# Optimization experiments

Hardware: AMD Instinct MI355X
Metric: run time of the kernel (lower is better)

## Reference

```python
import jax, jax.numpy as jnp
import numpy as np

B, T, E = 8, 1024, 512
H = 1024            # hidden_dim
NH, QD, VD = 4, 256, 512
C1, C2 = 512, 2     # conv1_out, conv2_out
K, PAD = 3, 1


def conv1d(x, w, b, pad):
    # x: [B, Cin, T], w: [Cout, Cin, K]
    y = jax.lax.conv_general_dilated(x, w, (1,), [(pad, pad)],
                                     dimension_numbers=('NCH', 'OIH', 'NCH'))
    return y + b[None, :, None]


def setup_inputs() -> dict:
    key = jax.random.key(0)
    ks = jax.random.split(key, 24)
    n = lambda i, shape, s=0.02: jax.random.normal(ks[i], shape, dtype=jnp.float32) * s
    inp = {
        'x':    jax.random.normal(ks[0], (B, T, E), dtype=jnp.float32),
        # in_pro: two 1x1 convs over channels (acting as linears)
        'w_in1': n(1, (E, E)), 'b_in1': jnp.zeros((E,), jnp.float32),
        'w_in2': n(2, (E, E)), 'b_in2': jnp.zeros((E,), jnp.float32),
        # attention projections
        'w_q': n(3, (NH * QD, E), float(np.sqrt(2.0 / (E + QD)))), 'b_q': jnp.zeros((NH * QD,), jnp.float32),
        'w_k': n(4, (NH * QD, E), float(np.sqrt(2.0 / (E + QD)))), 'b_k': jnp.zeros((NH * QD,), jnp.float32),
        'w_v': n(5, (NH * VD, E), float(np.sqrt(2.0 / (E + VD)))), 'b_v': jnp.zeros((NH * VD,), jnp.float32),
        # output projection (1x1 conv)
        'w_p': n(6, (E, NH * VD)), 'b_p': jnp.zeros((E,), jnp.float32),
        # layernorm
        'ln_g': jnp.ones((E,), jnp.float32), 'ln_b': jnp.zeros((E,), jnp.float32),
        # LSTM (1 layer, unidirectional, hidden H)
        'w_ih': n(7, (4 * H, E)), 'w_hh': n(8, (4 * H, H)),
        'b_ih': jnp.zeros((4 * H,), jnp.float32), 'b_hh': jnp.zeros((4 * H,), jnp.float32),
        # attention pooling convs
        'w_c1': n(9, (C1, H, K)), 'b_c1': jnp.zeros((C1,), jnp.float32),
        'w_c2': n(10, (C2, C1, K)), 'b_c2': jnp.zeros((C2,), jnp.float32),
    }
    return inp


def reference(x, w_in1, b_in1, w_in2, b_in2, w_q, b_q, w_k, b_k, w_v, b_v,
              w_p, b_p, ln_g, ln_b, w_ih, w_hh, b_ih, b_hh,
              w_c1, b_c1, w_c2, b_c2):
    # in_pro: 1x1 conv -> LeakyReLU(0.25) -> 1x1 conv (channel-wise linears)
    h = jnp.einsum('bte,fe->btf', x, w_in1) + b_in1
    h = jnp.where(h >= 0, h, 0.25 * h)
    h = jnp.einsum('bte,fe->btf', h, w_in2) + b_in2  # [B,T,E]

    # multi-head attention (no scale factor, as in the source)
    q = (jnp.einsum('bte,fe->btf', h, w_q) + b_q).reshape(B, T, NH, QD)
    k = (jnp.einsum('bte,fe->btf', h, w_k) + b_k).reshape(B, T, NH, QD)
    v = (jnp.einsum('bte,fe->btf', h, w_v) + b_v).reshape(B, T, NH, VD)
    scores = jnp.einsum('btnd,bsnd->bnts', q, k)          # [B,NH,T,T]
    attn = jax.nn.softmax(scores, axis=-1)
    o = jnp.einsum('bnts,bsnd->btnd', attn, v)            # [B,T,NH,VD]
    o = o.reshape(B, T, NH * VD)

    # p_conv1 (1x1) then LayerNorm over E
    y = jnp.einsum('btc,ec->bte', o, w_p) + b_p           # [B,T,E]
    mu = jnp.mean(y, axis=-1, keepdims=True)
    var = jnp.mean(jnp.square(y - mu), axis=-1, keepdims=True)
    y = (y - mu) * jax.lax.rsqrt(var + 1e-5) * ln_g + ln_b

    # LSTM (batch_first, 1 layer); dropout is identity in eval mode
    def step(carry, xt):
        hprev, cprev = carry
        g = xt @ w_ih.T + hprev @ w_hh.T + b_ih + b_hh    # [B,4H]
        i, f, gg, og = jnp.split(g, 4, axis=-1)
        c = jax.nn.sigmoid(f) * cprev + jax.nn.sigmoid(i) * jnp.tanh(gg)
        hn = jax.nn.sigmoid(og) * jnp.tanh(c)
        return (hn, c), hn
    init = (jnp.zeros((B, H), y.dtype), jnp.zeros((B, H), y.dtype))
    _, hs = jax.lax.scan(step, init, jnp.swapaxes(y, 0, 1))  # [T,B,H]
    lstm_out = jnp.swapaxes(hs, 0, 1)                        # [B,T,H]

    # conv-based attention pooling
    a = conv1d(jnp.swapaxes(lstm_out, 1, 2), w_c1, b_c1, PAD)  # [B,C1,T]
    a = jax.nn.relu(a)
    a = conv1d(a, w_c2, b_c2, PAD)                              # [B,C2,T]
    a = jax.nn.softmax(a, axis=2)
    feat = jnp.einsum('bct,bth->bch', a, lstm_out)              # [B,C2,H]
    return feat.reshape(B, C2 * H)
```

## Files before the change

### kernel.cpp

```cpp
#include <hip/hip_runtime.h>
#include <stdint.h>

typedef short short8 __attribute__((ext_vector_type(8)));
typedef short short4v __attribute__((ext_vector_type(4)));
typedef float float4v __attribute__((ext_vector_type(4)));

__device__ __forceinline__ float b2f(short s) {
    return __uint_as_float(((unsigned)(unsigned short)s) << 16);
}
__device__ __forceinline__ short f2b(float f) {
    unsigned u = __float_as_uint(f);
    unsigned r = (u + 0x7fffu + ((u >> 16) & 1u)) >> 16;
    return (short)r;
}

__global__ void k_prep_all(const float4v* __restrict__ xs,
                           const float4v* __restrict__ s0, const float4v* __restrict__ s1,
                           const float4v* __restrict__ s2, const float4v* __restrict__ s3,
                           const float4v* __restrict__ s4, const float4v* __restrict__ s5,
                           const float4v* __restrict__ s6, const float4v* __restrict__ s7,
                           short4v* __restrict__ xq, short4v* __restrict__ wq,
                           const float* __restrict__ wc1, short* __restrict__ wc1b,
                           const float* __restrict__ bih, const float* __restrict__ bhh,
                           float* __restrict__ bsum,
                           const float* __restrict__ bq, const float* __restrict__ bk,
                           const float* __restrict__ bv, float* __restrict__ bqkv,
                           short* __restrict__ lpad,
                           short* __restrict__ hs0, short* __restrict__ hs1,
                           int* __restrict__ arr, const float* __restrict__ bc2,
                           float* __restrict__ a2) {
    int t0 = blockIdx.x * blockDim.x + threadIdx.x;
    int stride = gridDim.x * blockDim.x;
    for (int i = t0; i < 3538944; i += stride) {
        float4v v;
        short4v* dst;
        int di;
        if (i < 1048576) { v = xs[i]; dst = xq; di = i; }
        else {
            int j = i - 1048576;
            dst = wq; di = j;
            if      (j <   65536) v = s0[j];
            else if (j <  131072) v = s1[j -   65536];
            else if (j <  262144) v = s2[j -  131072];
            else if (j <  393216) v = s3[j -  262144];
            else if (j <  655360) v = s4[j -  393216];
            else if (j <  917504) v = s5[j -  655360];
            else if (j < 1441792) v = s6[j -  917504];
            else                  v = s7[j - 1441792];
        }
        short4v o;
        o[0] = f2b(v[0]); o[1] = f2b(v[1]); o[2] = f2b(v[2]); o[3] = f2b(v[3]);
        dst[di] = o;
    }
    for (int i = t0; i < 512 * 3072; i += stride) {
        int c = i / 3072, rr = i % 3072, dk = rr / 1024, h = rr % 1024;
        wc1b[i] = f2b(wc1[(c * 1024 + h) * 3 + dk]);
    }
    for (int i = t0; i < 4096; i += stride) bsum[i] = bih[i] + bhh[i];
    for (int i = t0; i < 4096; i += stride) {
        float v;
        if (i < 1024) v = bq[i];
        else if (i < 2048) v = bk[i - 1024];
        else v = bv[i - 2048];
        bqkv[i] = v;
    }
    for (int i = t0; i < 16 * 1024; i += stride) {
        int b = i >> 11, r = (i >> 10) & 1, h = i & 1023;
        lpad[((long)(b * 1026 + r * 1025)) * 1024 + h] = 0;
    }
    for (int i = t0; i < 16384; i += stride) { hs0[i] = 0; hs1[i] = 0; }
    for (int i = t0; i < 64; i += stride) arr[i] = 0;
    for (int i = t0; i < 16384; i += stride) a2[i] = bc2[(i >> 10) & 1];
}

__global__ __launch_bounds__(256) void k_gemm_bt(
    const short* __restrict__ A, const short* __restrict__ B,
    float* __restrict__ Cf, short* __restrict__ Cb,
    const float* __restrict__ bias,
    int M, int N, int K, int lda, int ldb, int ldc,
    int z0n, long sA0, long sA1, long sB0, long sB1, long sC0, long sC1,
    int act, int gap, short* __restrict__ Cvt, int vtn0)
{
    __shared__ __align__(16) short lds[2 * 128 * 32];
    const int z = blockIdx.z;
    const int z0 = z % z0n, z1 = z / z0n;
    A += z1 * sA1 + z0 * sA0;
    B += z1 * sB1 + z0 * sB0;
    const long coff = z1 * sC1 + z0 * sC0;
    const int tn0 = blockIdx.x * 128, tm0 = blockIdx.y * 128;
    const int tid = threadIdx.x, ln = tid & 63, wv = tid >> 6;
    const int wr = wv >> 1, wc = wv & 1;

    const short* gbase[4];
    {
        const int gcol = (ln & 3) ^ ((ln >> 3) & 3);
#pragma unroll
        for (int j = 0; j < 4; ++j) {
            int c = wv * 4 + j;
            if (c < 8) {
                long grow = (long)(tm0 + c * 16 + (ln >> 2));
                if (gap) grow += 2 * (grow >> 10);
                gbase[j] = A + grow * (long)lda + gcol * 8;
            } else {
                gbase[j] = B + (long)(tn0 + (c - 8) * 16 + (ln >> 2)) * ldb + gcol * 8;
            }
        }
    }

    float4v acc[4][4];
#pragma unroll
    for (int i = 0; i < 4; ++i)
#pragma unroll
        for (int j = 0; j < 4; ++j) acc[i][j] = (float4v){0.f, 0.f, 0.f, 0.f};

    const int nk = K >> 5;
    for (int kt = 0; kt < nk; ++kt) {
        __syncthreads();
#pragma unroll
        for (int j = 0; j < 4; ++j) {
            int c = wv * 4 + j;
            __builtin_amdgcn_global_load_lds(
                (const __attribute__((address_space(1))) void*)(gbase[j] + kt * 32),
                (__attribute__((address_space(3))) void*)((short8*)lds + c * 64),
                16, 0, 0);
        }
        __syncthreads();

        short8 af[4], bf_[4];
        const int q = ln >> 4;
#pragma unroll
        for (int i = 0; i < 4; ++i) {
            int r = wr * 64 + i * 16 + (ln & 15);
            af[i] = ((short8*)lds)[r * 4 + (q ^ ((r >> 1) & 3))];
        }
#pragma unroll
        for (int j = 0; j < 4; ++j) {
            int r = wc * 64 + j * 16 + (ln & 15);
            bf_[j] = ((short8*)lds)[512 + r * 4 + (q ^ ((r >> 1) & 3))];
        }
#pragma unroll
        for (int i = 0; i < 4; ++i)
#pragma unroll
            for (int j = 0; j < 4; ++j)
                acc[i][j] = __builtin_amdgcn_mfma_f32_16x16x32_bf16(af[i], bf_[j], acc[i][j], 0, 0, 0);
    }

    if (Cvt && tn0 >= vtn0) {
#pragma unroll
        for (int j = 0; j < 4; ++j) {
            int nglob = tn0 + wc * 64 + j * 16 + (ln & 15);
            float bv = bias ? bias[nglob] : 0.f;
            int nv = nglob - vtn0;
            int nn = nv >> 9, d = nv & 511;
#pragma unroll
            for (int i = 0; i < 4; ++i) {
                int m0 = tm0 + wr * 64 + i * 16 + (ln >> 4) * 4;
                int b = m0 >> 10, s = m0 & 1023;
                short4v pk;
#pragma unroll
                for (int r = 0; r < 4; ++r) pk[r] = f2b(acc[i][j][r] + bv);
                *(short4v*)&Cvt[((long)((b * 4 + nn) * 512 + d)) * 1024 + s] = pk;
            }
        }
        return;
    }

#pragma unroll
    for (int j = 0; j < 4; ++j) {
        int nglob = tn0 + wc * 64 + j * 16 + (ln & 15);
        float bv = bias ? bias[nglob] : 0.f;
#pragma unroll
        for (int i = 0; i < 4; ++i) {
#pragma unroll
            for (int r = 0; r < 4; ++r) {
                int mglob = tm0 + wr * 64 + i * 16 + (ln >> 4) * 4 + r;
                float v = acc[i][j][r] + bv;
                if (act == 1) v = (v >= 0.f) ? v : 0.25f * v;
                else if (act == 2) v = fmaxf(v, 0.f);
                long ci = coff + (long)mglob * ldc + nglob;
                if (Cf) Cf[ci] = v;
                if (Cb) Cb[ci] = f2b(v);
            }
        }
    }
}

__global__ __launch_bounds__(256) void k_gemm_bt64(
    const short* __restrict__ A, const short* __restrict__ B,
    float* __restrict__ Cf, short* __restrict__ Cb,
    const float* __restrict__ bias,
    int M, int N, int K, int lda, int ldb, int ldc,
    int z0n, long sA0, long sA1, long sB0, long sB1, long sC0, long sC1,
    int act, int gap)
{
    __shared__ __align__(16) short lds[(64 + 128) * 32];
    const int z = blockIdx.z;
    const int z0 = z % z0n, z1 = z / z0n;
    A += z1 * sA1 + z0 * sA0;
    B += z1 * sB1 + z0 * sB0;
    const long coff = z1 * sC1 + z0 * sC0;
    const int tn0 = blockIdx.x * 128, tm0 = blockIdx.y * 64;
    const int tid = threadIdx.x, ln = tid & 63, wv = tid >> 6;
    const int wr = wv >> 1, wc = wv & 1;

    const short* gbase[3];
    {
        const int gcol = (ln & 3) ^ ((ln >> 3) & 3);
#pragma unroll
        for (int j = 0; j < 3; ++j) {
            int c = wv * 3 + j;
            if (c < 4) {
                long grow = (long)(tm0 + c * 16 + (ln >> 2));
                if (gap) grow += 2 * (grow >> 10);
                gbase[j] = A + grow * (long)lda + gcol * 8;
            } else {
                gbase[j] = B + (long)(tn0 + (c - 4) * 16 + (ln >> 2)) * ldb + gcol * 8;
            }
        }
    }

    float4v acc[2][4];
#pragma unroll
    for (int i = 0; i < 2; ++i)
#pragma unroll
        for (int j = 0; j < 4; ++j) acc[i][j] = (float4v){0.f, 0.f, 0.f, 0.f};

    const int nk = K >> 5;
    for (int kt = 0; kt < nk; ++kt) {
        __syncthreads();
#pragma unroll
        for (int j = 0; j < 3; ++j) {
            int c = wv * 3 + j;
            __builtin_amdgcn_global_load_lds(
                (const __attribute__((address_space(1))) void*)(gbase[j] + kt * 32),
                (__attribute__((address_space(3))) void*)((short8*)lds + c * 64),
                16, 0, 0);
        }
        __syncthreads();

        short8 af[2], bf_[4];
        const int q = ln >> 4;
#pragma unroll
        for (int i = 0; i < 2; ++i) {
            int r = wr * 32 + i * 16 + (ln & 15);
            af[i] = ((short8*)lds)[r * 4 + (q ^ ((r >> 1) & 3))];
        }
#pragma unroll
        for (int j = 0; j < 4; ++j) {
            int r = wc * 64 + j * 16 + (ln & 15);
            bf_[j] = ((short8*)lds)[256 + r * 4 + (q ^ ((r >> 1) & 3))];
        }
#pragma unroll
        for (int i = 0; i < 2; ++i)
#pragma unroll
            for (int j = 0; j < 4; ++j)
                acc[i][j] = __builtin_amdgcn_mfma_f32_16x16x32_bf16(af[i], bf_[j], acc[i][j], 0, 0, 0);
    }

#pragma unroll
    for (int j = 0; j < 4; ++j) {
        int nglob = tn0 + wc * 64 + j * 16 + (ln & 15);
        float bv = bias ? bias[nglob] : 0.f;
#pragma unroll
        for (int i = 0; i < 2; ++i) {
#pragma unroll
            for (int r = 0; r < 4; ++r) {
                int mglob = tm0 + wr * 32 + i * 16 + (ln >> 4) * 4 + r;
                float v = acc[i][j][r] + bv;
                if (act == 1) v = (v >= 0.f) ? v : 0.25f * v;
                else if (act == 2) v = fmaxf(v, 0.f);
                long ci = coff + (long)mglob * ldc + nglob;
                if (Cf) Cf[ci] = v;
                if (Cb) Cb[ci] = f2b(v);
            }
        }
    }
}

__global__ __launch_bounds__(256) void k_comb1(const float4v* __restrict__ p0,
                                               const float4v* __restrict__ p1,
                                               const float* __restrict__ bias,
                                               short4v* __restrict__ o) {
    int i = blockIdx.x * blockDim.x + threadIdx.x;
    int stride = gridDim.x * blockDim.x;
    for (; i < 1048576; i += stride) {
        float4v a = p0[i], b = p1[i];
        short4v r;
#pragma unroll
        for (int u = 0; u < 4; ++u) {
            float v = a[u] + b[u] + bias[(i * 4 + u) & 511];
            r[u] = f2b(fmaxf(v, 0.f));
        }
        o[i] = r;
    }
}

__global__ __launch_bounds__(256) void k_softmax_rows_bf16(short* __restrict__ p) {
    long row = blockIdx.x;
    short* r = p + (row << 10);
    int tid = threadIdx.x;
    float v[4];
    float mx = -3.4e38f;
#pragma unroll
    for (int i = 0; i < 4; ++i) { v[i] = b2f(r[tid + (i << 8)]); mx = fmaxf(mx, v[i]); }
#pragma unroll
    for (int d = 32; d > 0; d >>= 1) mx = fmaxf(mx, __shfl_down(mx, d));
    __shared__ float red[4], red2[4];
    if ((tid & 63) == 0) red[tid >> 6] = mx;
    __syncthreads();
    mx = fmaxf(fmaxf(red[0], red[1]), fmaxf(red[2], red[3]));
    float s = 0.f;
#pragma unroll
    for (int i = 0; i < 4; ++i) { v[i] = __expf(v[i] - mx); s += v[i]; }
#pragma unroll
    for (int d = 32; d > 0; d >>= 1) s += __shfl_down(s, d);
    if ((tid & 63) == 0) red2[tid >> 6] = s;
    __syncthreads();
    s = red2[0] + red2[1] + red2[2] + red2[3];
    float inv = 1.f / s;
#pragma unroll
    for (int i = 0; i < 4; ++i) r[tid + (i << 8)] = f2b(v[i] * inv);
}

__global__ __launch_bounds__(256) void k_layernorm(const short* __restrict__ y,
                                                   const float* __restrict__ gam,
                                                   const float* __restrict__ bet,
                                                   short* __restrict__ o) {
    const long row = blockIdx.x;
    const short* r = y + (row << 9);
    const int tid = threadIdx.x;
    float v0 = b2f(r[tid]), v1 = b2f(r[tid + 256]);
    float s = v0 + v1, ss = v0 * v0 + v1 * v1;
#pragma unroll
    for (int d = 32; d > 0; d >>= 1) { s += __shfl_down(s, d); ss += __shfl_down(ss, d); }
    __shared__ float rs_[4], rss[4];
    if ((tid & 63) == 0) { rs_[tid >> 6] = s; rss[tid >> 6] = ss; }
    __syncthreads();
    s = rs_[0] + rs_[1] + rs_[2] + rs_[3];
    ss = rss[0] + rss[1] + rss[2] + rss[3];
    float mean = s * (1.f / 512.f);
    float var = ss * (1.f / 512.f) - mean * mean;
    float rstd = rsqrtf(var + 1e-5f);
    short* out = o + (row << 9);
    out[tid]       = f2b((v0 - mean) * rstd * gam[tid]       + bet[tid]);
    out[tid + 256] = f2b((v1 - mean) * rstd * gam[tid + 256] + bet[tid + 256]);
}

__global__ __launch_bounds__(256) void k_lstm(
    const short* __restrict__ whh, const short* __restrict__ igb,
    short* __restrict__ hA, short* __restrict__ hB,
    short* __restrict__ lstm_pad, int* __restrict__ arr)
{
    const int g = blockIdx.x;
    const int tid = threadIdx.x;
    const int ln = tid & 63, wv = tid >> 6;
    const int kbase = wv * 256 + ((ln >> 4) << 3);
    const int arow = ln & 15;

    short8 wf[4][8];
#pragma unroll
    for (int q = 0; q < 4; ++q) {
        long row = (long)q * 1024 + g * 16 + (ln & 15);
#pragma unroll
        for (int kk = 0; kk < 8; ++kk)
            wf[q][kk] = *(const short8*)&whh[row * 1024 + kbase + kk * 32];
    }

    __shared__ float part[4][16][68];
    const int gm = tid >> 4, gu = tid & 15;
    float c_prev = 0.f;
    float igv[4];
    if (tid < 128) {
#pragma unroll
        for (int q = 0; q < 4; ++q)
            igv[q] = b2f(igb[((long)gm * 1024 + 0) * 4096 + q * 1024 + g * 16 + gu]);
    }

    for (int step = 0; step < 1024; ++step) {
        const short* hp = (step & 1) ? hB : hA;
        short8 af[8];
        if (arow < 8) {
            const unsigned long long* hq =
                (const unsigned long long*)(hp + arow * 1024 + kbase);
#pragma unroll
            for (int kk = 0; kk < 8; ++kk) {
                union { unsigned long long u[2]; short8 s; } cv;
                cv.u[0] = __hip_atomic_load(hq + kk * 8,     __ATOMIC_RELAXED, __HIP_MEMORY_SCOPE_AGENT);
                cv.u[1] = __hip_atomic_load(hq + kk * 8 + 1, __ATOMIC_RELAXED, __HIP_MEMORY_SCOPE_AGENT);
                af[kk] = cv.s;
            }
        } else {
#pragma unroll
            for (int kk = 0; kk < 8; ++kk) af[kk] = (short8){0, 0, 0, 0, 0, 0, 0, 0};
        }

        float4v acc[4];
#pragma unroll
        for (int q = 0; q < 4; ++q) acc[q] = (float4v){0.f, 0.f, 0.f, 0.f};
#pragma unroll
        for (int kk = 0; kk < 8; ++kk)
#pragma unroll
            for (int q = 0; q < 4; ++q)
                acc[q] = __builtin_amdgcn_mfma_f32_16x16x32_bf16(af[kk], wf[q][kk], acc[q], 0, 0, 0);

#pragma unroll
        for (int q = 0; q < 4; ++q)
#pragma unroll
            for (int rr = 0; rr < 4; ++rr)
                part[wv][(ln >> 4) * 4 + rr][q * 16 + (ln & 15)] = acc[q][rr];
        __syncthreads();

        if (tid < 128) {
            float psum[4];
#pragma unroll
            for (int q = 0; q < 4; ++q)
                psum[q] = part[0][gm][q * 16 + gu] + part[1][gm][q * 16 + gu]
                        + part[2][gm][q * 16 + gu] + part[3][gm][q * 16 + gu];
            float g0 = psum[0] + igv[0];
            float g1 = psum[1] + igv[1];
            float g2 = psum[2] + igv[2];
            float g3 = psum[3] + igv[3];
            float iv = 1.f / (1.f + __expf(-g0));
            float fv = 1.f / (1.f + __expf(-g1));
            float gv = 2.f / (1.f + __expf(-2.f * g2)) - 1.f;
            float ov = 1.f / (1.f + __expf(-g3));
            float c = fv * c_prev + iv * gv;
            c_prev = c;
            float h = ov * (2.f / (1.f + __expf(-2.f * c)) - 1.f);
            short hb16 = f2b(h);
            short* hn = (step & 1) ? hA : hB;
            __hip_atomic_store(&hn[gm * 1024 + g * 16 + gu], hb16,
                               __ATOMIC_RELAXED, __HIP_MEMORY_SCOPE_AGENT);
            lstm_pad[((long)gm * 1026 + step + 1) * 1024 + g * 16 + gu] = hb16;
        }

        __syncthreads();
        if (tid == 0)
            __hip_atomic_store(&arr[g], step + 1, __ATOMIC_RELAXED, __HIP_MEMORY_SCOPE_AGENT);
        if (tid < 128 && step + 1 < 1024) {
#pragma unroll
            for (int q = 0; q < 4; ++q)
                igv[q] = b2f(igb[((long)gm * 1024 + step + 1) * 4096 + q * 1024 + g * 16 + gu]);
        }
        if (wv == 0) {
            const int target = step + 1;
            long att = 0;
            while (true) {
                int f0 = __hip_atomic_load(&arr[ln], __ATOMIC_RELAXED, __HIP_MEMORY_SCOPE_AGENT);
                if (__all(f0 >= target)) break;
                if (++att > 20000000L) break;
                __builtin_amdgcn_s_sleep(1);
            }
        }
        __syncthreads();
    }
}

__global__ __launch_bounds__(256) void k_conv2(const short* __restrict__ a1,
                                               const float* __restrict__ w,
                                               float* __restrict__ a2,
                                               float* __restrict__ dz) {
    __shared__ float wl[384];
    int blk = blockIdx.x;
    int chunk = blk & 3, tq = (blk >> 2) & 3, bc = blk >> 4;
    int b = bc >> 1, c = bc & 1, t0 = tq * 256;
    int tid = threadIdx.x;
    int gid = blk * 256 + tid;
    if (gid < 16384) dz[gid] = 0.f;
    for (int i = tid; i < 384; i += 256) wl[i] = w[c * 1536 + chunk * 384 + i];
    __syncthreads();
    int t = t0 + tid;
    int j0 = chunk * 16;
    float s = 0.f;
    for (int dk = 0; dk < 3; ++dk) {
        int tt = t + dk - 1;
        if (tt < 0 || tt >= 1024) continue;
        const short8* arow = (const short8*)(a1 + (long)(b * 1024 + tt) * 512);
#pragma unroll 4
        for (int j = 0; j < 16; ++j) {
            short8 v = arow[j0 + j];
#pragma unroll
            for (int u = 0; u < 8; ++u)
                s += b2f(v[u]) * wl[(j * 8 + u) * 3 + dk];
        }
    }
    atomicAdd(&a2[(b * 2 + c) * 1024 + t], s);
}

__global__ __launch_bounds__(256) void k_feat(const float* __restrict__ a2,
                                              const short* __restrict__ lstm_pad,
                                              float* __restrict__ out) {
    int blk = blockIdx.x;
    int tc = blk & 3, qh = (blk >> 2) & 3, bc = blk >> 4;
    int b = bc >> 1;
    int tid = threadIdx.x;
    int h = qh * 256 + tid;
    __shared__ float aws[256];
    __shared__ float red[4], red2[4];
    float v[4];
    float mx = -3.4e38f;
#pragma unroll
    for (int i = 0; i < 4; ++i) { v[i] = a2[bc * 1024 + tid + (i << 8)]; mx = fmaxf(mx, v[i]); }
#pragma unroll
    for (int d = 32; d > 0; d >>= 1) mx = fmaxf(mx, __shfl_down(mx, d));
    if ((tid & 63) == 0) red[tid >> 6] = mx;
    __syncthreads();
    mx = fmaxf(fmaxf(red[0], red[1]), fmaxf(red[2], red[3]));
    float s = 0.f;
#pragma unroll
    for (int i = 0; i < 4; ++i) { v[i] = __expf(v[i] - mx); s += v[i]; }
#pragma unroll
    for (int d = 32; d > 0; d >>= 1) s += __shfl_down(s, d);
    if ((tid & 63) == 0) red2[tid >> 6] = s;
    __syncthreads();
    s = red2[0] + red2[1] + red2[2] + red2[3];
    float inv = 1.f / s;
    aws[tid] = v[tc] * inv;
    __syncthreads();
    float acc = 0.f;
#pragma unroll 16
    for (int j = 0; j < 256; ++j)
        acc += aws[j] * b2f(lstm_pad[((long)(b * 1026 + tc * 256 + j + 1)) * 1024 + h]);
    atomicAdd(&out[bc * 1024 + h], acc);
}

static void gemm_bt(hipStream_t st, const short* A, const short* B, float* Cf, short* Cb,
                    const float* bias, int M, int N, int K, int lda, int ldb, int ldc,
                    int z, int z0n, long sA0, long sA1, long sB0, long sB1, long sC0, long sC1,
                    int act, int gap, short* Cvt = nullptr, int vtn0 = 0) {
    dim3 grid(N / 128, M / 128, z);
    k_gemm_bt<<<grid, dim3(256), 0, st>>>(A, B, Cf, Cb, bias, M, N, K, lda, ldb, ldc,
                                          z0n, sA0, sA1, sB0, sB1, sC0, sC1, act, gap, Cvt, vtn0);
}

static void gemm_bt64(hipStream_t st, const short* A, const short* B, float* Cf, short* Cb,
                      const float* bias, int M, int N, int K, int lda, int ldb, int ldc,
                      int z, int z0n, long sA0, long sA1, long sB0, long sB1, long sC0, long sC1,
                      int act, int gap) {
    dim3 grid(N / 128, M / 64, z);
    k_gemm_bt64<<<grid, dim3(256), 0, st>>>(A, B, Cf, Cb, bias, M, N, K, lda, ldb, ldc,
                                            z0n, sA0, sA1, sB0, sB1, sC0, sC1, act, gap);
}

extern "C" void kernel_launch(void* const* d_in, const int* in_sizes, int n_in,
                              void* d_out, int out_size, void* d_ws, size_t ws_size,
                              hipStream_t stream) {
    if (ws_size < 199409920u) return;

    const float* x     = (const float*)d_in[0];
    const float* w_in1 = (const float*)d_in[1];
    const float* b_in1 = (const float*)d_in[2];
    const float* w_in2 = (const float*)d_in[3];
    const float* b_in2 = (const float*)d_in[4];
    const float* w_q   = (const float*)d_in[5];
    const float* b_q   = (const float*)d_in[6];
    const float* w_k   = (const float*)d_in[7];
    const float* b_k   = (const float*)d_in[8];
    const float* w_v   = (const float*)d_in[9];
    const float* b_v   = (const float*)d_in[10];
    const float* w_p   = (const float*)d_in[11];
    const float* b_p   = (const float*)d_in[12];
    const float* ln_g  = (const float*)d_in[13];
    const float* ln_b  = (const float*)d_in[14];
    const float* w_ih  = (const float*)d_in[15];
    const float* w_hh  = (const float*)d_in[16];
    const float* b_ih  = (const float*)d_in[17];
    const float* b_hh  = (const float*)d_in[18];
    const float* w_c1  = (const float*)d_in[19];
    const float* b_c1  = (const float*)d_in[20];
    const float* w_c2  = (const float*)d_in[21];
    const float* b_c2  = (const float*)d_in[22];

    char* ws = (char*)d_ws;
    short* w1b  = (short*)(ws + 0);
    short* w2b  = (short*)(ws + 524288);
    short* wqb  = (short*)(ws + 1048576);
    short* wpb  = (short*)(ws + 5242880);
    short* wihb = (short*)(ws + 7340032);
    short* whhb = (short*)(ws + 11534336);
    short* wc1b = (short*)(ws + 19922944);
    float* bsum = (float*)(ws + 23068672);
    short* hs0  = (short*)(ws + 23085056);
    short* hs1  = (short*)(ws + 23117824);
    int*   arr  = (int*)  (ws + 23150592);
    float* a2   = (float*)(ws + 23150848);
    short* lpad = (short*)(ws + 23216384);
    const size_t D0 = 40026368u;
    short* xbf   = (short*)(ws + D0);
    short* h1bf  = (short*)(ws + D0 + 8388608);
    short* h2bf  = (short*)(ws + D0 + 16777216);
    short* qkC   = (short*)(ws + D0 + 25165824);
    float* bqkv  = (float*)(ws + D0 + 58720256);
    short* vTbf  = (short*)(ws + D0 + 92274688);
    short* scb   = (short*)(ws + D0 + 58720256);
    short* obf   = (short*)(ws + D0 + 125829120);
    short* ybf   = (short*)(ws + D0 + 58720256);
    short* ylnbf = (short*)(ws + D0 + 67108864);
    short* igb   = (short*)(ws + D0 + 92274688);
    short* a1bf  = (short*)(ws + D0);
    float* cp0   = (float*)(ws + D0 + 8388608);
    float* cp1   = (float*)(ws + D0 + 25165824);

    k_prep_all<<<dim3(4096), dim3(256), 0, stream>>>(
        (const float4v*)x,
        (const float4v*)w_in1, (const float4v*)w_in2, (const float4v*)w_q, (const float4v*)w_k,
        (const float4v*)w_v, (const float4v*)w_p, (const float4v*)w_ih, (const float4v*)w_hh,
        (short4v*)xbf, (short4v*)w1b,
        w_c1, wc1b, b_ih, b_hh, bsum, b_q, b_k, b_v, bqkv,
        lpad, hs0, hs1, arr, b_c2, a2);

    gemm_bt64(stream, xbf, w1b, nullptr, h1bf, b_in1, 8192, 512, 512, 512, 512, 512,
              1, 1, 0, 0, 0, 0, 0, 0, 1, 0);
    gemm_bt64(stream, h1bf, w2b, nullptr, h2bf, b_in2, 8192, 512, 512, 512, 512, 512,
              1, 1, 0, 0, 0, 0, 0, 0, 0, 0);
    gemm_bt(stream, h2bf, wqb, nullptr, qkC, bqkv, 8192, 4096, 512, 512, 512, 2048,
            1, 1, 0, 0, 0, 0, 0, 0, 0, 0, vTbf, 2048);

    for (int bg = 0; bg < 2; ++bg) {
        const short* qb = qkC + (long)bg * 8388608;
        const short* kb = qkC + 1024 + (long)bg * 8388608;
        gemm_bt(stream, qb, kb, nullptr, scb, nullptr, 1024, 1024, 256, 2048, 2048, 1024,
                16, 4, 256, 2097152, 256, 2097152, 1048576, 4194304, 0, 0);
        k_softmax_rows_bf16<<<dim3(16384), dim3(256), 0, stream>>>(scb);
        gemm_bt64(stream, scb, vTbf + (long)bg * 8388608, nullptr, obf + (long)bg * 8388608, nullptr,
                  1024, 512, 1024, 1024, 1024, 2048,
                  16, 4, 1048576, 4194304, 524288, 2097152, 512, 2097152, 0, 0);
    }

    gemm_bt64(stream, obf, wpb, nullptr, ybf, b_p, 8192, 512, 2048, 2048, 2048, 512,
              1, 1, 0, 0, 0, 0, 0, 0, 0, 0);
    k_layernorm<<<dim3(8192), dim3(256), 0, stream>>>(ybf, ln_g, ln_b, ylnbf);
    gemm_bt(stream, ylnbf, wihb, nullptr, igb, bsum, 8192, 4096, 512, 512, 512, 4096,
            1, 1, 0, 0, 0, 0, 0, 0, 0, 0);
    k_lstm<<<dim3(64), dim3(256), 0, stream>>>(whhb, igb, hs0, hs1, lpad, arr);
    gemm_bt64(stream, lpad, wc1b, cp0, nullptr, nullptr, 8192, 512, 1536, 1024, 3072, 512,
              2, 2, 1536, 0, 1536, 0, 4194304, 0, 0, 1);
    k_comb1<<<dim3(4096), dim3(256), 0, stream>>>(
        (const float4v*)cp0, (const float4v*)cp1, b_c1, (short4v*)a1bf);
    k_conv2<<<dim3(256), dim3(256), 0, stream>>>(a1bf, w_c2, a2, (float*)d_out);
    k_feat<<<dim3(256), dim3(256), 0, stream>>>(a2, lpad, (float*)d_out);
    (void)in_sizes; (void)n_in; (void)out_size; (void)ws_size;
}
```

Measured before the change: 3.873 ms.

## Fuse conv1 GEMM into LSTM kernel, overlapping it with the recurrence

The LSTM recurrence kernel now also launches 512 extra blocks that compute the first pooling conv as a GEMM over the padded LSTM output. Each block spin-waits on a global step counter until its time rows are produced, so conv1 runs on idle CUs while the 64 sequential LSTM blocks are still working. The split-K partial buffers and the separate combine kernel are removed, with bias and ReLU folded into the GEMM epilogue. The risks are co-residency: waiting blocks could delay LSTM blocks from being scheduled, spin-wait timeouts could produce wrong results, and the extra memory traffic may slow the latency-bound recurrence.

```diff
diff --git a/kernel.cpp b/kernel.cpp
--- a/kernel.cpp
+++ b/kernel.cpp
@@ -277,24 +277,6 @@
     }
 }
 
-__global__ __launch_bounds__(256) void k_comb1(const float4v* __restrict__ p0,
-                                               const float4v* __restrict__ p1,
-                                               const float* __restrict__ bias,
-                                               short4v* __restrict__ o) {
-    int i = blockIdx.x * blockDim.x + threadIdx.x;
-    int stride = gridDim.x * blockDim.x;
-    for (; i < 1048576; i += stride) {
-        float4v a = p0[i], b = p1[i];
-        short4v r;
-#pragma unroll
-        for (int u = 0; u < 4; ++u) {
-            float v = a[u] + b[u] + bias[(i * 4 + u) & 511];
-            r[u] = f2b(fmaxf(v, 0.f));
-        }
-        o[i] = r;
-    }
-}
-
 __global__ __launch_bounds__(256) void k_softmax_rows_bf16(short* __restrict__ p) {
     long row = blockIdx.x;
     short* r = p + (row << 10);
@@ -346,113 +328,206 @@
     out[tid + 256] = f2b((v1 - mean) * rstd * gam[tid + 256] + bet[tid + 256]);
 }
 
-__global__ __launch_bounds__(256) void k_lstm(
+__global__ __launch_bounds__(256, 4) void k_lstm_c1(
     const short* __restrict__ whh, const short* __restrict__ igb,
     short* __restrict__ hA, short* __restrict__ hB,
-    short* __restrict__ lstm_pad, int* __restrict__ arr)
+    short* __restrict__ lstm_pad, int* __restrict__ arr,
+    const short* __restrict__ wc1b, const float* __restrict__ bc1,
+    short* __restrict__ a1bf)
 {
-    const int g = blockIdx.x;
-    const int tid = threadIdx.x;
-    const int ln = tid & 63, wv = tid >> 6;
-    const int kbase = wv * 256 + ((ln >> 4) << 3);
-    const int arow = ln & 15;
-
-    short8 wf[4][8];
-#pragma unroll
-    for (int q = 0; q < 4; ++q) {
-        long row = (long)q * 1024 + g * 16 + (ln & 15);
-#pragma unroll
-        for (int kk = 0; kk < 8; ++kk)
-            wf[q][kk] = *(const short8*)&whh[row * 1024 + kbase + kk * 32];
-    }
-
     __shared__ float part[4][16][68];
-    const int gm = tid >> 4, gu = tid & 15;
-    float c_prev = 0.f;
-    float igv[4];
-    if (tid < 128) {
-#pragma unroll
-        for (int q = 0; q < 4; ++q)
-            igv[q] = b2f(igb[((long)gm * 1024 + 0) * 4096 + q * 1024 + g * 16 + gu]);
-    }
-
-    for (int step = 0; step < 1024; ++step) {
-        const short* hp = (step & 1) ? hB : hA;
-        short8 af[8];
-        if (arow < 8) {
-            const unsigned long long* hq =
-                (const unsigned long long*)(hp + arow * 1024 + kbase);
-#pragma unroll
-            for (int kk = 0; kk < 8; ++kk) {
-                union { unsigned long long u[2]; short8 s; } cv;
-                cv.u[0] = __hip_atomic_load(hq + kk * 8,     __ATOMIC_RELAXED, __HIP_MEMORY_SCOPE_AGENT);
-                cv.u[1] = __hip_atomic_load(hq + kk * 8 + 1, __ATOMIC_RELAXED, __HIP_MEMORY_SCOPE_AGENT);
-                af[kk] = cv.s;
-            }
-        } else {
-#pragma unroll
-            for (int kk = 0; kk < 8; ++kk) af[kk] = (short8){0, 0, 0, 0, 0, 0, 0, 0};
-        }
-
-        float4v acc[4];
-#pragma unroll
-        for (int q = 0; q < 4; ++q) acc[q] = (float4v){0.f, 0.f, 0.f, 0.f};
-#pragma unroll
-        for (int kk = 0; kk < 8; ++kk)
+    __shared__ __align__(16) short clds[(64 + 128) * 32];
+    int* gstep = (int*)(hA + 16000);
+
+    if (blockIdx.x < 64) {
+        const int g = blockIdx.x;
+        const int tid = threadIdx.x;
+        const int ln = tid & 63, wv = tid >> 6;
+        const int kbase = wv * 256 + ((ln >> 4) << 3);
+        const int arow = ln & 15;
+
+        short8 wf[4][8];
+#pragma unroll
+        for (int q = 0; q < 4; ++q) {
+            long row = (long)q * 1024 + g * 16 + (ln & 15);
+#pragma unroll
+            for (int kk = 0; kk < 8; ++kk)
+                wf[q][kk] = *(const short8*)&whh[row * 1024 + kbase + kk * 32];
+        }
+
+        const int gm = tid >> 4, gu = tid & 15;
+        float c_prev = 0.f;
+        float igv[4];
+        if (tid < 128) {
 #pragma unroll
             for (int q = 0; q < 4; ++q)
-                acc[q] = __builtin_amdgcn_mfma_f32_16x16x32_bf16(af[kk], wf[q][kk], acc[q], 0, 0, 0);
-
-#pragma unroll
-        for (int q = 0; q < 4; ++q)
-#pragma unroll
-            for (int rr = 0; rr < 4; ++rr)
-                part[wv][(ln >> 4) * 4 + rr][q * 16 + (ln & 15)] = acc[q][rr];
+                igv[q] = b2f(igb[((long)gm * 1024 + 0) * 4096 + q * 1024 + g * 16 + gu]);
+        }
+
+        for (int step = 0; step < 1024; ++step) {
+            const short* hp = (step & 1) ? hB : hA;
+            short8 af[8];
+            if (arow < 8) {
+                const unsigned long long* hq =
+                    (const unsigned long long*)(hp + arow * 1024 + kbase);
+#pragma unroll
+                for (int kk = 0; kk < 8; ++kk) {
+                    union { unsigned long long u[2]; short8 s; } cv;
+                    cv.u[0] = __hip_atomic_load(hq + kk * 8,     __ATOMIC_RELAXED, __HIP_MEMORY_SCOPE_AGENT);
+                    cv.u[1] = __hip_atomic_load(hq + kk * 8 + 1, __ATOMIC_RELAXED, __HIP_MEMORY_SCOPE_AGENT);
+                    af[kk] = cv.s;
+                }
+            } else {
+#pragma unroll
+                for (int kk = 0; kk < 8; ++kk) af[kk] = (short8){0, 0, 0, 0, 0, 0, 0, 0};
+            }
+
+            float4v acc[4];
+#pragma unroll
+            for (int q = 0; q < 4; ++q) acc[q] = (float4v){0.f, 0.f, 0.f, 0.f};
+#pragma unroll
+            for (int kk = 0; kk < 8; ++kk)
+#pragma unroll
+                for (int q = 0; q < 4; ++q)
+                    acc[q] = __builtin_amdgcn_mfma_f32_16x16x32_bf16(af[kk], wf[q][kk], acc[q], 0, 0, 0);
+
+#pragma unroll
+            for (int q = 0; q < 4; ++q)
+#pragma unroll
+                for (int rr = 0; rr < 4; ++rr)
+                    part[wv][(ln >> 4) * 4 + rr][q * 16 + (ln & 15)] = acc[q][rr];
+            __syncthreads();
+
+            if (tid < 128) {
+                float psum[4];
+#pragma unroll
+                for (int q = 0; q < 4; ++q)
+                    psum[q] = part[0][gm][q * 16 + gu] + part[1][gm][q * 16 + gu]
+                            + part[2][gm][q * 16 + gu] + part[3][gm][q * 16 + gu];
+                float g0 = psum[0] + igv[0];
+                float g1 = psum[1] + igv[1];
+                float g2 = psum[2] + igv[2];
+                float g3 = psum[3] + igv[3];
+                float iv = 1.f / (1.f + __expf(-g0));
+                float fv = 1.f / (1.f + __expf(-g1));
+                float gv = 2.f / (1.f + __expf(-2.f * g2)) - 1.f;
+                float ov = 1.f / (1.f + __expf(-g3));
+                float c = fv * c_prev + iv * gv;
+                c_prev = c;
+                float h = ov * (2.f / (1.f + __expf(-2.f * c)) - 1.f);
+                short hb16 = f2b(h);
+                short* hn = (step & 1) ? hA : hB;
+                __hip_atomic_store(&hn[gm * 1024 + g * 16 + gu], hb16,
+                                   __ATOMIC_RELAXED, __HIP_MEMORY_SCOPE_AGENT);
+                __hip_atomic_store(&lstm_pad[((long)gm * 1026 + step + 1) * 1024 + g * 16 + gu],
+                                   hb16, __ATOMIC_RELAXED, __HIP_MEMORY_SCOPE_AGENT);
+            }
+
+            __syncthreads();
+            if (tid == 0)
+                __hip_atomic_store(&arr[g], step + 1, __ATOMIC_RELAXED, __HIP_MEMORY_SCOPE_AGENT);
+            if (tid < 128 && step + 1 < 1024) {
+#pragma unroll
+                for (int q = 0; q < 4; ++q)
+                    igv[q] = b2f(igb[((long)gm * 1024 + step + 1) * 4096 + q * 1024 + g * 16 + gu]);
+            }
+            if (wv == 0) {
+                const int target = step + 1;
+                long att = 0;
+                while (true) {
+                    int f0 = __hip_atomic_load(&arr[ln], __ATOMIC_RELAXED, __HIP_MEMORY_SCOPE_AGENT);
+                    if (__all(f0 >= target)) break;
+                    if (++att > 20000000L) break;
+                    __builtin_amdgcn_s_sleep(1);
+                }
+                if (g == 0 && ln == 0)
+                    __hip_atomic_store(gstep, target, __ATOMIC_RELAXED, __HIP_MEMORY_SCOPE_AGENT);
+            }
+            __syncthreads();
+        }
+    } else {
+        const int cb = (int)blockIdx.x - 64;
+        const int tn0 = (cb & 3) * 128, tm0 = (cb >> 2) * 64;
+        if (threadIdx.x == 0) {
+            const int thr0 = (tm0 & 1023) + 65;
+            const int thr = thr0 < 1024 ? thr0 : 1024;
+            long att = 0;
+            while (__hip_atomic_load(gstep, __ATOMIC_RELAXED, __HIP_MEMORY_SCOPE_AGENT) < thr) {
+                if (++att > 2000000L) break;
+                __builtin_amdgcn_s_sleep(32);
+            }
+        }
         __syncthreads();
 
-        if (tid < 128) {
-            float psum[4];
-#pragma unroll
-            for (int q = 0; q < 4; ++q)
-                psum[q] = part[0][gm][q * 16 + gu] + part[1][gm][q * 16 + gu]
-                        + part[2][gm][q * 16 + gu] + part[3][gm][q * 16 + gu];
-            float g0 = psum[0] + igv[0];
-            float g1 = psum[1] + igv[1];
-            float g2 = psum[2] + igv[2];
-            float g3 = psum[3] + igv[3];
-            float iv = 1.f / (1.f + __expf(-g0));
-            float fv = 1.f / (1.f + __expf(-g1));
-            float gv = 2.f / (1.f + __expf(-2.f * g2)) - 1.f;
-            float ov = 1.f / (1.f + __expf(-g3));
-            float c = fv * c_prev + iv * gv;
-            c_prev = c;
-            float h = ov * (2.f / (1.f + __expf(-2.f * c)) - 1.f);
-            short hb16 = f2b(h);
-            short* hn = (step & 1) ? hA : hB;
-            __hip_atomic_store(&hn[gm * 1024 + g * 16 + gu], hb16,
-                               __ATOMIC_RELAXED, __HIP_MEMORY_SCOPE_AGENT);
-            lstm_pad[((long)gm * 1026 + step + 1) * 1024 + g * 16 + gu] = hb16;
-        }
-
-        __syncthreads();
-        if (tid == 0)
-            __hip_atomic_store(&arr[g], step + 1, __ATOMIC_RELAXED, __HIP_MEMORY_SCOPE_AGENT);
-        if (tid < 128 && step + 1 < 1024) {
-#pragma unroll
-            for (int q = 0; q < 4; ++q)
-                igv[q] = b2f(igb[((long)gm * 1024 + step + 1) * 4096 + q * 1024 + g * 16 + gu]);
-        }
-        if (wv == 0) {
-            const int target = step + 1;
-            long att = 0;
-            while (true) {
-                int f0 = __hip_atomic_load(&arr[ln], __ATOMIC_RELAXED, __HIP_MEMORY_SCOPE_AGENT);
-                if (__all(f0 >= target)) break;
-                if (++att > 20000000L) break;
-                __builtin_amdgcn_s_sleep(1);
-            }
-        }
-        __syncthreads();
+        const int tid = threadIdx.x, ln = tid & 63, wv = tid >> 6;
+        const int wr = wv >> 1, wc = wv & 1;
+        const short* gbase[3];
+        {
+            const int gcol = (ln & 3) ^ ((ln >> 3) & 3);
+#pragma unroll
+            for (int j = 0; j < 3; ++j) {
+                int c = wv * 3 + j;
+                if (c < 4) {
+                    long grow = (long)(tm0 + c * 16 + (ln >> 2));
+                    grow += 2 * (grow >> 10);
+                    gbase[j] = lstm_pad + grow * 1024L + gcol * 8;
+                } else {
+                    gbase[j] = wc1b + (long)(tn0 + (c - 4) * 16 + (ln >> 2)) * 3072 + gcol * 8;
+                }
+            }
+        }
+
+        float4v acc[2][4];
+#pragma unroll
+        for (int i = 0; i < 2; ++i)
+#pragma unroll
+            for (int j = 0; j < 4; ++j) acc[i][j] = (float4v){0.f, 0.f, 0.f, 0.f};
+
+        for (int kt = 0; kt < 96; ++kt) {
+            __syncthreads();
+#pragma unroll
+            for (int j = 0; j < 3; ++j) {
+                int c = wv * 3 + j;
+                __builtin_amdgcn_global_load_lds(
+                    (const __attribute__((address_space(1))) void*)(gbase[j] + kt * 32),
+                    (__attribute__((address_space(3))) void*)((short8*)clds + c * 64),
+                    16, 0, 0);
+            }
+            __syncthreads();
+
+            short8 af[2], bf_[4];
+            const int q = ln >> 4;
+#pragma unroll
+            for (int i = 0; i < 2; ++i) {
+                int r = wr * 32 + i * 16 + (ln & 15);
+                af[i] = ((short8*)clds)[r * 4 + (q ^ ((r >> 1) & 3))];
+            }
+#pragma unroll
+            for (int j = 0; j < 4; ++j) {
+                int r = wc * 64 + j * 16 + (ln & 15);
+                bf_[j] = ((short8*)clds)[256 + r * 4 + (q ^ ((r >> 1) & 3))];
+            }
+#pragma unroll
+            for (int i = 0; i < 2; ++i)
+#pragma unroll
+                for (int j = 0; j < 4; ++j)
+                    acc[i][j] = __builtin_amdgcn_mfma_f32_16x16x32_bf16(af[i], bf_[j], acc[i][j], 0, 0, 0);
+        }
+
+#pragma unroll
+        for (int j = 0; j < 4; ++j) {
+            int nglob = tn0 + wc * 64 + j * 16 + (ln & 15);
+            float bv = bc1[nglob];
+#pragma unroll
+            for (int i = 0; i < 2; ++i) {
+#pragma unroll
+                for (int r = 0; r < 4; ++r) {
+                    int mglob = tm0 + wr * 32 + i * 16 + (ln >> 4) * 4 + r;
+                    float v = fmaxf(acc[i][j][r] + bv, 0.f);
+                    a1bf[(long)mglob * 512 + nglob] = f2b(v);
+                }
+            }
+        }
     }
 }
 
@@ -598,8 +673,6 @@
     short* ylnbf = (short*)(ws + D0 + 67108864);
     short* igb   = (short*)(ws + D0 + 92274688);
     short* a1bf  = (short*)(ws + D0);
-    float* cp0   = (float*)(ws + D0 + 8388608);
-    float* cp1   = (float*)(ws + D0 + 25165824);
 
     k_prep_all<<<dim3(4096), dim3(256), 0, stream>>>(
         (const float4v*)x,
@@ -632,11 +705,8 @@
     k_layernorm<<<dim3(8192), dim3(256), 0, stream>>>(ybf, ln_g, ln_b, ylnbf);
     gemm_bt(stream, ylnbf, wihb, nullptr, igb, bsum, 8192, 4096, 512, 512, 512, 4096,
             1, 1, 0, 0, 0, 0, 0, 0, 0, 0);
-    k_lstm<<<dim3(64), dim3(256), 0, stream>>>(whhb, igb, hs0, hs1, lpad, arr);
-    gemm_bt64(stream, lpad, wc1b, cp0, nullptr, nullptr, 8192, 512, 1536, 1024, 3072, 512,
-              2, 2, 1536, 0, 1536, 0, 4194304, 0, 0, 1);
-    k_comb1<<<dim3(4096), dim3(256), 0, stream>>>(
-        (const float4v*)cp0, (const float4v*)cp1, b_c1, (short4v*)a1bf);
+    k_lstm_c1<<<dim3(576), dim3(256), 0, stream>>>(whhb, igb, hs0, hs1, lpad, arr,
+                                                   wc1b, b_c1, a1bf);
     k_conv2<<<dim3(256), dim3(256), 0, stream>>>(a1bf, w_c2, a2, (float*)d_out);
     k_feat<<<dim3(256), dim3(256), 0, stream>>>(a2, lpad, (float*)d_out);
     (void)in_sizes; (void)n_in; (void)out_size; (void)ws_size;
```

Result: slower. 6.395 ms (+65.1%).

## Halve LSTM persistent grid by giving each block 32 hidden units

Applied to the files above, without the earlier changes.

The persistent LSTM kernel now runs on 32 workgroups instead of 64, with each one holding register-resident W_hh fragments for 32 hidden units (twice as many MFMA tiles per step). All 256 threads now do the gate math instead of half. The aim is to cut the cost of the per-step cross-block barrier, since fewer blocks poll the arrival flags and fewer flags have to be gathered. In exchange, each step does twice the MFMA work per block and weight-register pressure doubles, which could cause spills or lower the clock-level parallelism.

```diff
diff --git a/kernel.cpp b/kernel.cpp
--- a/kernel.cpp
+++ b/kernel.cpp
@@ -357,24 +357,24 @@
     const int kbase = wv * 256 + ((ln >> 4) << 3);
     const int arow = ln & 15;
 
-    short8 wf[4][8];
-#pragma unroll
-    for (int q = 0; q < 4; ++q) {
-        long row = (long)q * 1024 + g * 16 + (ln & 15);
-#pragma unroll
-        for (int kk = 0; kk < 8; ++kk)
-            wf[q][kk] = *(const short8*)&whh[row * 1024 + kbase + kk * 32];
-    }
-
-    __shared__ float part[4][16][68];
-    const int gm = tid >> 4, gu = tid & 15;
+    short8 wf[4][2][8];
+#pragma unroll
+    for (int q = 0; q < 4; ++q)
+#pragma unroll
+        for (int u2 = 0; u2 < 2; ++u2) {
+            long row = (long)q * 1024 + g * 32 + u2 * 16 + (ln & 15);
+#pragma unroll
+            for (int kk = 0; kk < 8; ++kk)
+                wf[q][u2][kk] = *(const short8*)&whh[row * 1024 + kbase + kk * 32];
+        }
+
+    __shared__ float part[4][16][132];
+    const int gm = tid >> 5, gu = tid & 31;
     float c_prev = 0.f;
     float igv[4];
-    if (tid < 128) {
-#pragma unroll
-        for (int q = 0; q < 4; ++q)
-            igv[q] = b2f(igb[((long)gm * 1024 + 0) * 4096 + q * 1024 + g * 16 + gu]);
-    }
+#pragma unroll
+    for (int q = 0; q < 4; ++q)
+        igv[q] = b2f(igb[((long)gm * 1024 + 0) * 4096 + q * 1024 + g * 32 + gu]);
 
     for (int step = 0; step < 1024; ++step) {
         const short* hp = (step & 1) ? hB : hA;
@@ -394,28 +394,34 @@
             for (int kk = 0; kk < 8; ++kk) af[kk] = (short8){0, 0, 0, 0, 0, 0, 0, 0};
         }
 
-        float4v acc[4];
-#pragma unroll
-        for (int q = 0; q < 4; ++q) acc[q] = (float4v){0.f, 0.f, 0.f, 0.f};
+        float4v acc[4][2];
+#pragma unroll
+        for (int q = 0; q < 4; ++q)
+#pragma unroll
+            for (int u2 = 0; u2 < 2; ++u2) acc[q][u2] = (float4v){0.f, 0.f, 0.f, 0.f};
 #pragma unroll
         for (int kk = 0; kk < 8; ++kk)
 #pragma unroll
+            for (int q = 0; q < 4; ++q) {
+                acc[q][0] = __builtin_amdgcn_mfma_f32_16x16x32_bf16(af[kk], wf[q][0][kk], acc[q][0], 0, 0, 0);
+                acc[q][1] = __builtin_amdgcn_mfma_f32_16x16x32_bf16(af[kk], wf[q][1][kk], acc[q][1], 0, 0, 0);
+            }
+
+#pragma unroll
+        for (int q = 0; q < 4; ++q)
+#pragma unroll
+            for (int u2 = 0; u2 < 2; ++u2)
+#pragma unroll
+                for (int rr = 0; rr < 4; ++rr)
+                    part[wv][(ln >> 4) * 4 + rr][q * 32 + u2 * 16 + (ln & 15)] = acc[q][u2][rr];
+        __syncthreads();
+
+        {
+            float psum[4];
+#pragma unroll
             for (int q = 0; q < 4; ++q)
-                acc[q] = __builtin_amdgcn_mfma_f32_16x16x32_bf16(af[kk], wf[q][kk], acc[q], 0, 0, 0);
-
-#pragma unroll
-        for (int q = 0; q < 4; ++q)
-#pragma unroll
-            for (int rr = 0; rr < 4; ++rr)
-                part[wv][(ln >> 4) * 4 + rr][q * 16 + (ln & 15)] = acc[q][rr];
-        __syncthreads();
-
-        if (tid < 128) {
-            float psum[4];
-#pragma unroll
-            for (int q = 0; q < 4; ++q)
-                psum[q] = part[0][gm][q * 16 + gu] + part[1][gm][q * 16 + gu]
-                        + part[2][gm][q * 16 + gu] + part[3][gm][q * 16 + gu];
+                psum[q] = part[0][gm][q * 32 + gu] + part[1][gm][q * 32 + gu]
+                        + part[2][gm][q * 32 + gu] + part[3][gm][q * 32 + gu];
             float g0 = psum[0] + igv[0];
             float g1 = psum[1] + igv[1];
             float g2 = psum[2] + igv[2];
@@ -429,24 +435,26 @@
             float h = ov * (2.f / (1.f + __expf(-2.f * c)) - 1.f);
             short hb16 = f2b(h);
             short* hn = (step & 1) ? hA : hB;
-            __hip_atomic_store(&hn[gm * 1024 + g * 16 + gu], hb16,
+            __hip_atomic_store(&hn[gm * 1024 + g * 32 + gu], hb16,
                                __ATOMIC_RELAXED, __HIP_MEMORY_SCOPE_AGENT);
-            lstm_pad[((long)gm * 1026 + step + 1) * 1024 + g * 16 + gu] = hb16;
+            lstm_pad[((long)gm * 1026 + step + 1) * 1024 + g * 32 + gu] = hb16;
         }
 
         __syncthreads();
         if (tid == 0)
             __hip_atomic_store(&arr[g], step + 1, __ATOMIC_RELAXED, __HIP_MEMORY_SCOPE_AGENT);
-        if (tid < 128 && step + 1 < 1024) {
+        if (step + 1 < 1024) {
 #pragma unroll
             for (int q = 0; q < 4; ++q)
-                igv[q] = b2f(igb[((long)gm * 1024 + step + 1) * 4096 + q * 1024 + g * 16 + gu]);
+                igv[q] = b2f(igb[((long)gm * 1024 + step + 1) * 4096 + q * 1024 + g * 32 + gu]);
         }
         if (wv == 0) {
             const int target = step + 1;
             long att = 0;
             while (true) {
-                int f0 = __hip_atomic_load(&arr[ln], __ATOMIC_RELAXED, __HIP_MEMORY_SCOPE_AGENT);
+                int f0 = target;
+                if (ln < 32)
+                    f0 = __hip_atomic_load(&arr[ln], __ATOMIC_RELAXED, __HIP_MEMORY_SCOPE_AGENT);
                 if (__all(f0 >= target)) break;
                 if (++att > 20000000L) break;
                 __builtin_amdgcn_s_sleep(1);
@@ -632,7 +640,7 @@
     k_layernorm<<<dim3(8192), dim3(256), 0, stream>>>(ybf, ln_g, ln_b, ylnbf);
     gemm_bt(stream, ylnbf, wihb, nullptr, igb, bsum, 8192, 4096, 512, 512, 512, 4096,
             1, 1, 0, 0, 0, 0, 0, 0, 0, 0);
-    k_lstm<<<dim3(64), dim3(256), 0, stream>>>(whhb, igb, hs0, hs1, lpad, arr);
+    k_lstm<<<dim3(32), dim3(256), 0, stream>>>(whhb, igb, hs0, hs1, lpad, arr);
     gemm_bt64(stream, lpad, wc1b, cp0, nullptr, nullptr, 8192, 512, 1536, 1024, 3072, 512,
               2, 2, 1536, 0, 1536, 0, 4194304, 0, 0, 1);
     k_comb1<<<dim3(4096), dim3(256), 0, stream>>>(
```

Result: slower. 4.234 ms (+9.3%).
